# Kernel tuning notes

Hardware: AMD Instinct MI355X
Metric: run time of the kernel (lower is better)

The kernel has to match this reference:

```python
import jax, jax.numpy as jnp
import numpy as np

D = 512
K = 32
B = 2
L = 2048


def setup_inputs() -> dict:
    key = jax.random.key(0)
    ks = jax.random.split(key, 12)
    s = 1.0 / np.sqrt(D)
    return {
        "x": jax.random.normal(ks[0], (B, L, D), dtype=jnp.float32),
        "W1": jax.random.normal(ks[1], (D, D), dtype=jnp.float32) * s,
        "b1": jnp.zeros((D,), jnp.float32),
        "W2": jax.random.normal(ks[2], (D, K), dtype=jnp.float32) * s,
        "b2": jnp.zeros((K,), jnp.float32),
        "pos_scale": jnp.array([0.5], jnp.float32),
        "content_scale": jnp.array([0.5], jnp.float32),
        "Wv": jax.random.normal(ks[3], (D, D), dtype=jnp.float32) * s,
        "bv": jnp.zeros((D,), jnp.float32),
        "ln_g": jnp.ones((D,), jnp.float32),
        "ln_b": jnp.zeros((D,), jnp.float32),
        "Wo": jax.random.normal(ks[4], (D, D), dtype=jnp.float32) * s,
        "bo": jnp.zeros((D,), jnp.float32),
    }


def reference(x, W1, b1, W2, b2, pos_scale, content_scale, Wv, bv, ln_g, ln_b, Wo, bo):
    Bb, Ll, Dd = x.shape
    Kk = W2.shape[1]
    # fixed positional phases: outer(positions, 1/10000^(k/K))
    freqs = 1.0 / (10000.0 ** (jnp.arange(Kk, dtype=jnp.float32) / Kk))
    pos_phase = jnp.arange(Ll, dtype=jnp.float32)[:, None] * freqs[None, :]  # [L,K]
    # content phase: Linear -> Tanh -> Linear, then tanh * pi
    h = jnp.tanh(x @ W1 + b1)
    content_phase = jnp.tanh(h @ W2 + b2) * jnp.pi  # [B,L,K]
    total_phase = pos_scale * pos_phase[None] + content_scale * content_phase  # [B,L,K]
    value = x @ Wv + bv  # [B,L,D]
    c = jnp.cos(total_phase)
    s = jnp.sin(total_phase)
    # phasor outer-product bind: [B,L,K,D]
    bound_real = c[..., None] * value[:, :, None, :]
    bound_imag = s[..., None] * value[:, :, None, :]
    mem_real = jnp.cumsum(bound_real, axis=1)
    mem_imag = jnp.cumsum(bound_imag, axis=1)
    retrieved = (mem_real * c[..., None] + mem_imag * s[..., None]).sum(axis=2)  # [B,L,D]
    norm = jnp.sqrt(jnp.arange(1, Ll + 1, dtype=jnp.float32) * Kk)[None, :, None]
    retrieved = retrieved / norm
    # to_out: LayerNorm then Linear
    mu = retrieved.mean(axis=-1, keepdims=True)
    var = retrieved.var(axis=-1, keepdims=True)
    ln = (retrieved - mu) / jnp.sqrt(var + 1e-5) * ln_g + ln_b
    return x + ln @ Wo + bo
```

## Files before the change

### kernel.cpp

```cpp
#include <hip/hip_runtime.h>
#include <hip/hip_bf16.h>
#include <math.h>

#define BB   2
#define LL   2048
#define DD   512
#define KK   32
#define BL   (BB*LL)
#define NCH  64

typedef unsigned short ushort_t;
typedef __bf16 bf16x8 __attribute__((ext_vector_type(8)));
typedef float  f32x4  __attribute__((ext_vector_type(4)));
typedef unsigned short ushort8 __attribute__((ext_vector_type(8)));

__device__ __forceinline__ void gl_lds16(const void* g, void* l) {
    __builtin_amdgcn_global_load_lds(
        (const __attribute__((address_space(1))) void*)g,
        (__attribute__((address_space(3))) void*)l, 16, 0, 0);
}
__device__ __forceinline__ ushort_t f2b(float f) {
    __bf16 b = (__bf16)f; return *(ushort_t*)&b;
}
__device__ __forceinline__ float b2f(ushort_t u) {
    unsigned int x = ((unsigned int)u) << 16; return *(float*)&x;
}

__global__ __launch_bounds__(256) void prep(const float* __restrict__ W1,
                                            const float* __restrict__ Wv,
                                            const float* __restrict__ Wo,
                                            const float* __restrict__ W2,
                                            const float* __restrict__ x,
                                            const float* __restrict__ lng,
                                            const float* __restrict__ lnb,
                                            const float* __restrict__ bo,
                                            __hip_bfloat16* __restrict__ Wct,
                                            __hip_bfloat16* __restrict__ Wot,
                                            __hip_bfloat16* __restrict__ W2T,
                                            __hip_bfloat16* __restrict__ xb,
                                            float* __restrict__ U,
                                            float* __restrict__ VBc)
{
    __shared__ float tile[32][33];
    const int bz = blockIdx.z;
    const int tx = threadIdx.x, ty = threadIdx.y;
    const int t = ty * 32 + tx;

    if (bz == 3) {
        const int bid = blockIdx.y * 16 + blockIdx.x;
        const float4* src = (const float4*)x + (size_t)bid * 2048 + t;
        ushort4* dst = (ushort4*)xb + (size_t)bid * 2048 + t;
        #pragma unroll
        for (int i = 0; i < 8; ++i) {
            float4 v = src[i * 256];
            ushort4 o = {f2b(v.x), f2b(v.y), f2b(v.z), f2b(v.w)};
            dst[i * 256] = o;
        }
        return;
    }
    if (bz == 4) {
        if (blockIdx.x != 0) return;
        const int kg = blockIdx.y;
        const int k0 = kg * 32;
        float u0 = 0.f, u1 = 0.f, v0 = 0.f, v1 = 0.f;
        #pragma unroll 4
        for (int k = 0; k < 32; ++k) {
            const float g1 = lng[k0 + k], b1v = lnb[k0 + k];
            const float w0 = Wo[(size_t)(k0 + k) * 512 + t];
            const float w1 = Wo[(size_t)(k0 + k) * 512 + t + 256];
            u0 = fmaf(g1, w0, u0);  u1 = fmaf(g1, w1, u1);
            v0 = fmaf(b1v, w0, v0); v1 = fmaf(b1v, w1, v1);
        }
        if (kg == 0) { v0 += bo[t]; v1 += bo[t + 256]; }
        atomicAdd(&U[t], u0);         atomicAdd(&U[t + 256], u1);
        atomicAdd(&VBc[t], v0);       atomicAdd(&VBc[t + 256], v1);
        return;
    }
    if (bz == 5) {
        if (blockIdx.x != 0) return;
        const int r0 = blockIdx.y * 32;
        #pragma unroll
        for (int i = 0; i < 4; ++i)
            tile[ty + 8 * i][tx] = W2[(size_t)(r0 + ty + 8 * i) * 32 + tx];
        __syncthreads();
        #pragma unroll
        for (int i = 0; i < 4; ++i)
            W2T[(size_t)(ty + 8 * i) * 512 + r0 + tx] =
                __float2bfloat16(tile[tx][ty + 8 * i]);
        return;
    }
    const float* src = bz == 0 ? W1 : (bz == 1 ? Wv : Wo);
    __hip_bfloat16* dst = bz == 0 ? Wct
                        : (bz == 1 ? Wct + 512 * 512 : Wot);
    const int r0 = blockIdx.y * 32, c0 = blockIdx.x * 32;
    #pragma unroll
    for (int i = 0; i < 4; ++i)
        tile[ty + 8 * i][tx] = src[(size_t)(r0 + ty + 8 * i) * 512 + c0 + tx];
    __syncthreads();
    const float sc = (bz == 2) ? lng[r0 + tx] : 1.f;
    #pragma unroll
    for (int i = 0; i < 4; ++i)
        dst[(size_t)(c0 + ty + 8 * i) * 512 + r0 + tx] =
            __float2bfloat16(tile[tx][ty + 8 * i] * sc);
}

template<int BM, int MODE>
__global__ __launch_bounds__(256) void gemm_mfma(
    const ushort_t* __restrict__ A, const ushort_t* __restrict__ Bt,
    const float* __restrict__ bias0, const float* __restrict__ bias1,
    const float* __restrict__ resid,
    __hip_bfloat16* __restrict__ outH, __hip_bfloat16* __restrict__ outV,
    float* __restrict__ outF, const float* __restrict__ stats)
{
    constexpr int WROWS = BM / 2;
    constexpr int MF    = WROWS / 16;
    constexpr int ACH   = BM / 32;
    __shared__ __align__(16) ushort_t As[BM * 64];
    __shared__ __align__(16) ushort_t Bs[128 * 64];
    __shared__ float muL[BM], rsL[BM];

    const int t  = threadIdx.x;
    const int m0 = blockIdx.y * BM, n0 = blockIdx.x * 128;
    const int l  = t & 63, w = t >> 6;
    const int wr = w >> 1, wc = w & 1;
    const int l15 = l & 15, hi = l >> 4;

    if (MODE == 1 && t < BM) {
        float4 st = *(const float4*)(stats + (size_t)(m0 + t) * 4);
        float s = st.x + st.z, s2 = st.y + st.w;
        float mu = s * (1.f / 512), var = s2 * (1.f / 512) - mu * mu;
        muL[t] = mu;
        rsL[t] = rsqrtf(var + 1e-5f);
    }

    const ushort_t* agp[ACH];
    const ushort_t* bgp[4];
    #pragma unroll
    for (int i = 0; i < ACH; ++i) {
        int row = (t >> 3) + 32 * i, slot = (t & 7) ^ (row & 7);
        agp[i] = A + (size_t)(m0 + row) * 512 + slot * 8;
    }
    #pragma unroll
    for (int i = 0; i < 4; ++i) {
        int row = (t >> 3) + 32 * i, slot = (t & 7) ^ (row & 7);
        bgp[i] = Bt + (size_t)(n0 + row) * 512 + slot * 8;
    }

    int aoff[MF][2], boff[4][2];
    #pragma unroll
    for (int mi = 0; mi < MF; ++mi)
        #pragma unroll
        for (int kh = 0; kh < 2; ++kh) {
            int row = wr * WROWS + mi * 16 + l15;
            aoff[mi][kh] = row * 128 + (((kh * 4 + hi) ^ (row & 7)) * 16);
        }
    #pragma unroll
    for (int nj = 0; nj < 4; ++nj)
        #pragma unroll
        for (int kh = 0; kh < 2; ++kh) {
            int row = wc * 64 + nj * 16 + l15;
            boff[nj][kh] = row * 128 + (((kh * 4 + hi) ^ (row & 7)) * 16);
        }

    f32x4 acc[MF][4];
    #pragma unroll
    for (int mi = 0; mi < MF; ++mi)
        #pragma unroll
        for (int nj = 0; nj < 4; ++nj)
            acc[mi][nj] = f32x4{0.f, 0.f, 0.f, 0.f};

    for (int k0 = 0; k0 < 512; k0 += 64) {
        __syncthreads();
        #pragma unroll
        for (int i = 0; i < ACH; ++i)
            gl_lds16(agp[i] + k0, (char*)As + (size_t)(i * 256 + t) * 16);
        #pragma unroll
        for (int i = 0; i < 4; ++i)
            gl_lds16(bgp[i] + k0, (char*)Bs + (size_t)(i * 256 + t) * 16);
        __syncthreads();
        #pragma unroll
        for (int kh = 0; kh < 2; ++kh) {
            bf16x8 af[MF], bfr[4];
            #pragma unroll
            for (int mi = 0; mi < MF; ++mi)
                af[mi] = *(const bf16x8*)((const char*)As + aoff[mi][kh]);
            #pragma unroll
            for (int nj = 0; nj < 4; ++nj)
                bfr[nj] = *(const bf16x8*)((const char*)Bs + boff[nj][kh]);
            #pragma unroll
            for (int mi = 0; mi < MF; ++mi)
                #pragma unroll
                for (int nj = 0; nj < 4; ++nj)
                    acc[mi][nj] = __builtin_amdgcn_mfma_f32_16x16x32_bf16(
                        af[mi], bfr[nj], acc[mi][nj], 0, 0, 0);
        }
    }

    #pragma unroll
    for (int nj = 0; nj < 4; ++nj) {
        const int gcol = n0 + wc * 64 + nj * 16 + l15;
        if (MODE == 0) {
            const float bsv = (gcol < 512) ? bias0[gcol] : bias1[gcol - 512];
            #pragma unroll
            for (int mi = 0; mi < MF; ++mi)
                #pragma unroll
                for (int r = 0; r < 4; ++r) {
                    const int grow = m0 + wr * WROWS + mi * 16 + hi * 4 + r;
                    float v = acc[mi][nj][r] + bsv;
                    if (gcol < 512)
                        outH[(size_t)grow * 512 + gcol] = __float2bfloat16(tanhf(v));
                    else
                        outV[(size_t)grow * 512 + (gcol - 512)] = __float2bfloat16(v);
                }
        } else {
            const float uN = bias0[gcol], vbN = bias1[gcol];
            #pragma unroll
            for (int mi = 0; mi < MF; ++mi)
                #pragma unroll
                for (int r = 0; r < 4; ++r) {
                    const int rl = wr * WROWS + mi * 16 + hi * 4 + r;
                    const int grow = m0 + rl;
                    const float rs = rsL[rl], mu = muL[rl];
                    outF[(size_t)grow * 512 + gcol] =
                        resid[(size_t)grow * 512 + gcol]
                        + rs * acc[mi][nj][r] - rs * mu * uN + vbN;
                }
        }
    }
}

__global__ __launch_bounds__(256) void scanA(const __hip_bfloat16* __restrict__ Vb,
                                             const __hip_bfloat16* __restrict__ Hb,
                                             const __hip_bfloat16* __restrict__ W2T,
                                             const float* __restrict__ b2,
                                             const float* __restrict__ ps_p,
                                             const float* __restrict__ cs_p,
                                             float* __restrict__ Ca,
                                             float* __restrict__ Sa,
                                             ushort_t* __restrict__ PPg)
{
    __shared__ __align__(16) ushort_t regA[32 * 520];
    __shared__ __align__(16) ushort_t regB[32 * 520];
    ushort_t* Hs  = regA;
    ushort_t* VT  = regA;
    ushort_t* CT  = regA + 256 * 40;
    ushort_t* ST  = regA + 256 * 40 + 32 * 40;
    ushort_t* W2L = regB;
    ushort_t* PPs = regB;

    const int t = threadIdx.x;
    const int bch = blockIdx.x, dh = blockIdx.y;
    const int b = bch >> 6, ch = bch & 63;
    const size_t vbase = ((size_t)b * LL + ch * 32) * DD + dh * 256;
    const int w = t >> 6, l = t & 63, l15 = l & 15, hi = l >> 4;

    {
        const ushort8* hsrc = (const ushort8*)((const ushort_t*)Hb
                               + ((size_t)b * LL + ch * 32) * DD);
        const ushort8* wsrc = (const ushort8*)((const ushort_t*)W2T);
        #pragma unroll
        for (int i = 0; i < 8; ++i) {
            const int id = i * 256 + t;
            const int row = id >> 6, c8 = id & 63;
            ushort8 hv = hsrc[id];
            ushort8 wv = wsrc[id];
            *(ushort8*)&Hs[row * 520 + c8 * 8] = hv;
            *(ushort8*)&W2L[row * 520 + c8 * 8] = wv;
        }
    }
    __syncthreads();

    f32x4 pacc[2][2];
    #pragma unroll
    for (int mt = 0; mt < 2; ++mt)
        #pragma unroll
        for (int nt = 0; nt < 2; ++nt)
            pacc[mt][nt] = f32x4{0.f,0.f,0.f,0.f};
    for (int ks = 0; ks < 16; ++ks) {
        bf16x8 af[2], bfr[2];
        #pragma unroll
        for (int mt = 0; mt < 2; ++mt)
            af[mt] = *(const bf16x8*)&Hs[(16 * mt + l15) * 520 + ks * 32 + hi * 8];
        #pragma unroll
        for (int nt = 0; nt < 2; ++nt)
            bfr[nt] = *(const bf16x8*)&W2L[(16 * nt + l15) * 520 + ks * 32 + hi * 8];
        #pragma unroll
        for (int mt = 0; mt < 2; ++mt)
            #pragma unroll
            for (int nt = 0; nt < 2; ++nt)
                pacc[mt][nt] = __builtin_amdgcn_mfma_f32_16x16x32_bf16(
                    af[mt], bfr[nt], pacc[mt][nt], 0, 0, 0);
    }
    __syncthreads();

    {
        const float psv = ps_p[0], csv = cs_p[0];
        #pragma unroll
        for (int nt = 0; nt < 2; ++nt) {
            const int kk = l15 + 16 * nt;
            const float freq = exp2f(-(float)kk * (13.287712379549449f / (float)KK));
            const float b2k = b2[kk];
            #pragma unroll
            for (int mt = 0; mt < 2; ++mt) {
                ushort_t cw[4], sw[4];
                #pragma unroll
                for (int r = 0; r < 4; ++r) {
                    const int lloc = 16 * mt + hi * 4 + r;
                    const int lpos = ch * 32 + lloc;
                    const float content = tanhf(pacc[mt][nt][r] + b2k)
                                          * 3.14159265358979323846f * csv;
                    const float total = psv * ((float)lpos * freq) + content;
                    float sv, cv;
                    sincosf(total, &sv, &cv);
                    cw[r] = f2b(cv); sw[r] = f2b(sv);
                    if (dh == 0) {
                        const size_t gi = ((size_t)b * LL + lpos) * KK + kk;
                        Ca[gi] = cv; Sa[gi] = sv;
                    }
                }
                *(ushort4*)&CT[kk * 40 + 16 * mt + hi * 4] = *(ushort4*)cw;
                *(ushort4*)&ST[kk * 40 + 16 * mt + hi * 4] = *(ushort4*)sw;
            }
        }
    }
    {
        const int lg = t >> 5, dg = t & 31;
        ushort8 r[4];
        #pragma unroll
        for (int i = 0; i < 4; ++i)
            r[i] = *(const ushort8*)((const ushort_t*)Vb + vbase
                                     + (size_t)(lg * 4 + i) * DD + dg * 8);
        #pragma unroll
        for (int jd = 0; jd < 8; ++jd) {
            ushort4 w4 = {r[0][jd], r[1][jd], r[2][jd], r[3][jd]};
            *(ushort4*)&VT[(dg * 8 + jd) * 40 + lg * 4] = w4;
        }
    }
    __syncthreads();

    bf16x8 afc[2], afs[2];
    #pragma unroll
    for (int mt = 0; mt < 2; ++mt) {
        afc[mt] = *(const bf16x8*)&CT[(l15 + 16 * mt) * 40 + hi * 8];
        afs[mt] = *(const bf16x8*)&ST[(l15 + 16 * mt) * 40 + hi * 8];
    }
    f32x4 aPR[2][4], aPI[2][4];
    #pragma unroll
    for (int mt = 0; mt < 2; ++mt)
        #pragma unroll
        for (int nt = 0; nt < 4; ++nt) {
            aPR[mt][nt] = f32x4{0.f,0.f,0.f,0.f};
            aPI[mt][nt] = f32x4{0.f,0.f,0.f,0.f};
        }
    #pragma unroll
    for (int nt = 0; nt < 4; ++nt) {
        bf16x8 bv = *(const bf16x8*)&VT[(w * 64 + nt * 16 + l15) * 40 + hi * 8];
        #pragma unroll
        for (int mt = 0; mt < 2; ++mt) {
            aPR[mt][nt] = __builtin_amdgcn_mfma_f32_16x16x32_bf16(afc[mt], bv, aPR[mt][nt], 0,0,0);
            aPI[mt][nt] = __builtin_amdgcn_mfma_f32_16x16x32_bf16(afs[mt], bv, aPI[mt][nt], 0,0,0);
        }
    }
    #pragma unroll
    for (int mt = 0; mt < 2; ++mt)
        #pragma unroll
        for (int nt = 0; nt < 4; ++nt) {
            const int dloc = w * 64 + nt * 16 + l15;
            const int kq = 16 * mt + hi * 4;
            const int oR = kq >> 3, oI = 4 + (kq >> 3);
            const int sub = (hi & 1) * 4;
            ushort4 pr4 = {f2b(aPR[mt][nt][0]), f2b(aPR[mt][nt][1]),
                           f2b(aPR[mt][nt][2]), f2b(aPR[mt][nt][3])};
            ushort4 pi4 = {f2b(aPI[mt][nt][0]), f2b(aPI[mt][nt][1]),
                           f2b(aPI[mt][nt][2]), f2b(aPI[mt][nt][3])};
            *(ushort4*)&PPs[dloc * 64 + ((oR ^ (dloc & 7)) * 8) + sub] = pr4;
            *(ushort4*)&PPs[dloc * 64 + ((oI ^ (dloc & 7)) * 8) + sub] = pi4;
        }
    __syncthreads();
    ushort_t* gout = PPg + ((size_t)bch * 512 + dh * 256) * 64;
    #pragma unroll
    for (int i = 0; i < 8; ++i)
        *(ushort8*)(gout + (size_t)(i * 256 + t) * 8) =
            *(const ushort8*)&PPs[(i * 256 + t) * 8];
}

__global__ __launch_bounds__(256) void scan_prefix(ushort_t* __restrict__ PPg)
{
    const int g = blockIdx.x * 256 + threadIdx.x;
    const int b = g >> 15, p = g & 32767;
    float run = 0.f;
    for (int gg = 0; gg < 4; ++gg) {
        ushort_t v[16];
        #pragma unroll
        for (int i = 0; i < 16; ++i)
            v[i] = PPg[(size_t)(b * 64 + gg * 16 + i) * 32768 + p];
        #pragma unroll
        for (int i = 0; i < 16; ++i) {
            ushort_t o = f2b(run);
            run += b2f(v[i]);
            PPg[(size_t)(b * 64 + gg * 16 + i) * 32768 + p] = o;
        }
    }
}

__global__ __launch_bounds__(256) void scanC(__hip_bfloat16* Vb,
                                             const float* __restrict__ Ca,
                                             const float* __restrict__ Sa,
                                             const ushort_t* __restrict__ PPg,
                                             float* __restrict__ StatsG)
{
    __shared__ __align__(16) ushort_t VT[256 * 40];
    __shared__ __align__(16) ushort_t PPT[256 * 64];
    __shared__ __align__(16) ushort_t CS[32 * 80];
    __shared__ __align__(16) ushort_t G[32 * 40];
    __shared__ __align__(16) ushort_t RT[4][32 * 64];
    __shared__ float2 statsL[4][32];

    const int t = threadIdx.x;
    const int bch = blockIdx.x, dh = blockIdx.y;
    const int b = bch >> 6, ch = bch & 63;
    const size_t vbase = ((size_t)b * LL + ch * 32) * DD + dh * 256;

    {
        const ushort_t* ppg = PPg + ((size_t)bch * 512 + dh * 256) * 64;
        #pragma unroll
        for (int i = 0; i < 8; ++i)
            gl_lds16(ppg + (size_t)(i * 256 + t) * 8,
                     (char*)PPT + (size_t)(i * 256 + t) * 16);
    }
    {
        const int lg = t >> 5, dg = t & 31;
        ushort8 r[4];
        #pragma unroll
        for (int i = 0; i < 4; ++i)
            r[i] = *(const ushort8*)((const ushort_t*)Vb + vbase
                                     + (size_t)(lg * 4 + i) * DD + dg * 8);
        #pragma unroll
        for (int jd = 0; jd < 8; ++jd) {
            ushort4 w4 = {r[0][jd], r[1][jd], r[2][jd], r[3][jd]};
            *(ushort4*)&VT[(dg * 8 + jd) * 40 + lg * 4] = w4;
        }
    }
    {
        const int half = t >> 7;
        const int tt = t & 127;
        const int lrow = tt >> 2, kq = tt & 3;
        const float* srcp = half ? Sa : Ca;
        float4 v0 = *(const float4*)(srcp + ((size_t)b * LL + ch * 32 + lrow) * KK + kq * 8);
        float4 v1 = *(const float4*)(srcp + ((size_t)b * LL + ch * 32 + lrow) * KK + kq * 8 + 4);
        ushort8 w8 = {f2b(v0.x), f2b(v0.y), f2b(v0.z), f2b(v0.w),
                      f2b(v1.x), f2b(v1.y), f2b(v1.z), f2b(v1.w)};
        *(ushort8*)&CS[lrow * 80 + half * 32 + kq * 8] = w8;
    }
    __syncthreads();

    const int w = t >> 6, l = t & 63, l15 = l & 15, hi = l >> 4;

    {
        bf16x8 fc[2], fs[2];
        #pragma unroll
        for (int mt = 0; mt < 2; ++mt) {
            fc[mt] = *(const bf16x8*)&CS[(l15 + 16 * mt) * 80 + hi * 8];
            fs[mt] = *(const bf16x8*)&CS[(l15 + 16 * mt) * 80 + 32 + hi * 8];
        }
        f32x4 gacc[2][2];
        #pragma unroll
        for (int mt = 0; mt < 2; ++mt)
            #pragma unroll
            for (int nt = 0; nt < 2; ++nt) {
                gacc[mt][nt] = f32x4{0.f,0.f,0.f,0.f};
                gacc[mt][nt] = __builtin_amdgcn_mfma_f32_16x16x32_bf16(fc[mt], fc[nt], gacc[mt][nt], 0,0,0);
                gacc[mt][nt] = __builtin_amdgcn_mfma_f32_16x16x32_bf16(fs[mt], fs[nt], gacc[mt][nt], 0,0,0);
            }
        #pragma unroll
        for (int mt = 0; mt < 2; ++mt)
            #pragma unroll
            for (int nt = 0; nt < 2; ++nt)
                #pragma unroll
                for (int r = 0; r < 4; ++r) {
                    const int row = 16 * mt + hi * 4 + r;
                    const int col = 16 * nt + l15;
                    float gv = (col <= row) ? gacc[mt][nt][r] : 0.f;
                    G[row * 40 + col] = f2b(gv);
                }
    }

    bf16x8 a1[2][2], ag[2];
    #pragma unroll
    for (int mt = 0; mt < 2; ++mt) {
        a1[mt][0] = *(const bf16x8*)&CS[(l15 + 16 * mt) * 80 + hi * 8];
        a1[mt][1] = *(const bf16x8*)&CS[(l15 + 16 * mt) * 80 + 32 + hi * 8];
        ag[mt]    = *(const bf16x8*)&G[(l15 + 16 * mt) * 40 + hi * 8];
    }
    f32x4 acc[2][4];
    #pragma unroll
    for (int mt = 0; mt < 2; ++mt)
        #pragma unroll
        for (int nt = 0; nt < 4; ++nt)
            acc[mt][nt] = f32x4{0.f,0.f,0.f,0.f};
    #pragma unroll
    for (int nt = 0; nt < 4; ++nt) {
        const int drow = w * 64 + nt * 16 + l15;
        bf16x8 bp0 = *(const bf16x8*)((const char*)PPT + drow * 128 + ((hi ^ (drow & 7)) << 4));
        bf16x8 bp1 = *(const bf16x8*)((const char*)PPT + drow * 128 + (((4 + hi) ^ (drow & 7)) << 4));
        bf16x8 bv  = *(const bf16x8*)&VT[drow * 40 + hi * 8];
        #pragma unroll
        for (int mt = 0; mt < 2; ++mt) {
            acc[mt][nt] = __builtin_amdgcn_mfma_f32_16x16x32_bf16(a1[mt][0], bp0, acc[mt][nt], 0,0,0);
            acc[mt][nt] = __builtin_amdgcn_mfma_f32_16x16x32_bf16(a1[mt][1], bp1, acc[mt][nt], 0,0,0);
            acc[mt][nt] = __builtin_amdgcn_mfma_f32_16x16x32_bf16(ag[mt],    bv,  acc[mt][nt], 0,0,0);
        }
    }

    float sP[2][4] = {}, qP[2][4] = {};
    #pragma unroll
    for (int mt = 0; mt < 2; ++mt)
        #pragma unroll
        for (int nt = 0; nt < 4; ++nt)
            #pragma unroll
            for (int r = 0; r < 4; ++r) {
                const int lrow = 16 * mt + hi * 4 + r;
                const float scale = rsqrtf((float)((ch * 32 + lrow + 1) * KK));
                const float val = acc[mt][nt][r] * scale;
                sP[mt][r] += val;
                qP[mt][r] = fmaf(val, val, qP[mt][r]);
                RT[w][lrow * 64 + nt * 16 + l15] = f2b(val);
            }
    #pragma unroll
    for (int c = 0; c < 4; ++c) {
        const int cid = c * 64 + l;
        const int row = cid >> 3, c8 = cid & 7;
        ushort8 v = *(const ushort8*)&RT[w][row * 64 + c8 * 8];
        *(ushort8*)((ushort_t*)Vb + ((size_t)b * LL + ch * 32 + row) * DD
                    + dh * 256 + w * 64 + c8 * 8) = v;
    }
    #pragma unroll
    for (int mt = 0; mt < 2; ++mt)
        #pragma unroll
        for (int r = 0; r < 4; ++r) {
            float sv = sP[mt][r], qv = qP[mt][r];
            #pragma unroll
            for (int off = 1; off < 16; off <<= 1) {
                sv += __shfl_xor(sv, off);
                qv += __shfl_xor(qv, off);
            }
            if (l15 == 0)
                statsL[w][16 * mt + hi * 4 + r] = float2{sv, qv};
        }
    __syncthreads();
    if (t < 32) {
        float s = 0.f, q = 0.f;
        #pragma unroll
        for (int w4 = 0; w4 < 4; ++w4) {
            float2 p = statsL[w4][t];
            s += p.x; q += p.y;
        }
        const size_t rowg = (size_t)b * LL + ch * 32 + t;
        *(float2*)&StatsG[(rowg * 2 + dh) * 2] = float2{s, q};
    }
}

extern "C" void kernel_launch(void* const* d_in, const int* in_sizes, int n_in,
                              void* d_out, int out_size, void* d_ws, size_t ws_size,
                              hipStream_t stream)
{
    const float* x   = (const float*)d_in[0];
    const float* W1  = (const float*)d_in[1];
    const float* b1  = (const float*)d_in[2];
    const float* W2  = (const float*)d_in[3];
    const float* b2  = (const float*)d_in[4];
    const float* ps  = (const float*)d_in[5];
    const float* cs  = (const float*)d_in[6];
    const float* Wv  = (const float*)d_in[7];
    const float* bv  = (const float*)d_in[8];
    const float* lng = (const float*)d_in[9];
    const float* lnb = (const float*)d_in[10];
    const float* Wo  = (const float*)d_in[11];
    const float* bo  = (const float*)d_in[12];
    float* out = (float*)d_out;

    char* wsb = (char*)d_ws;
    __hip_bfloat16* Vb  = (__hip_bfloat16*)(wsb);
    ushort_t* PPg = (ushort_t*)(wsb + (4u << 20));
    float* Ca  = (float*)(wsb + (12u << 20));
    float* Sa  = (float*)(wsb + (12u << 20) + (512u << 10));
    __hip_bfloat16* xb  = (__hip_bfloat16*)(wsb + (13u << 20));
    __hip_bfloat16* Hb  = (__hip_bfloat16*)(wsb + (17u << 20));
    __hip_bfloat16* Wct = (__hip_bfloat16*)(wsb + (21u << 20));
    __hip_bfloat16* Wot = (__hip_bfloat16*)(wsb + (22u << 20));
    float* StatsG = (float*)(wsb + (23u << 20));
    float* U      = (float*)(wsb + (23u << 20) + (64u << 10));
    float* VBc    = (float*)(wsb + (23u << 20) + (66u << 10));
    __hip_bfloat16* W2T = (__hip_bfloat16*)(wsb + (23u << 20) + (68u << 10));

    hipMemsetAsync(U, 0, 4096, stream);
    prep<<<dim3(16, 16, 6), dim3(32, 8), 0, stream>>>(
        W1, Wv, Wo, W2, x, lng, lnb, bo, Wct, Wot, W2T, xb, U, VBc);
    gemm_mfma<64, 0><<<dim3(8, 64), dim3(256), 0, stream>>>(
        (const ushort_t*)xb, (const ushort_t*)Wct, b1, bv, nullptr, Hb, Vb, nullptr, nullptr);
    scanA<<<dim3(BB * NCH, 2), dim3(256), 0, stream>>>(
        Vb, Hb, W2T, b2, ps, cs, Ca, Sa, PPg);
    scan_prefix<<<dim3(256), dim3(256), 0, stream>>>(PPg);
    scanC<<<dim3(BB * NCH, 2), dim3(256), 0, stream>>>(Vb, Ca, Sa, PPg, StatsG);
    gemm_mfma<64, 1><<<dim3(4, 64), dim3(256), 0, stream>>>(
        (const ushort_t*)Vb, (const ushort_t*)Wot, U, VBc, x, nullptr, nullptr, out, StatsG);
}
```

Before: 63.67 us.

## Drop memset and atomics, store cos/sin as swizzled bf16, shrink output GEMM tile

The LayerNorm-folded bias vectors are now written as per-group partials and summed inside the output GEMM, which removes the hipMemsetAsync launch and the atomic adds. The cos/sin phases go from scanA to scanC as a pre-swizzled bf16 block that is copied straight into LDS with global_load_lds, instead of two fp32 arrays that needed reloading and converting. The final GEMM switches from 64-row to 32-row tiles, doubling the block count. In exchange, every output GEMM block re-reads 16 partial vectors, and the smaller tiles reuse each loaded Wo tile less.

Result: faster. 59.91 us (-5.9%).

```diff
diff --git a/kernel.cpp b/kernel.cpp
--- a/kernel.cpp
+++ b/kernel.cpp
@@ -38,8 +38,8 @@
                                             __hip_bfloat16* __restrict__ Wot,
                                             __hip_bfloat16* __restrict__ W2T,
                                             __hip_bfloat16* __restrict__ xb,
-                                            float* __restrict__ U,
-                                            float* __restrict__ VBc)
+                                            float* __restrict__ Upart,
+                                            float* __restrict__ Vpart)
 {
     __shared__ float tile[32][33];
     const int bz = blockIdx.z;
@@ -72,8 +72,8 @@
             v0 = fmaf(b1v, w0, v0); v1 = fmaf(b1v, w1, v1);
         }
         if (kg == 0) { v0 += bo[t]; v1 += bo[t + 256]; }
-        atomicAdd(&U[t], u0);         atomicAdd(&U[t + 256], u1);
-        atomicAdd(&VBc[t], v0);       atomicAdd(&VBc[t + 256], v1);
+        Upart[kg * 512 + t] = u0;       Upart[kg * 512 + t + 256] = u1;
+        Vpart[kg * 512 + t] = v0;       Vpart[kg * 512 + t + 256] = v1;
         return;
     }
     if (bz == 5) {
@@ -117,7 +117,7 @@
     constexpr int ACH   = BM / 32;
     __shared__ __align__(16) ushort_t As[BM * 64];
     __shared__ __align__(16) ushort_t Bs[128 * 64];
-    __shared__ float muL[BM], rsL[BM];
+    __shared__ float muL[BM], rsL[BM], uL[128], vbL[128];
 
     const int t  = threadIdx.x;
     const int m0 = blockIdx.y * BM, n0 = blockIdx.x * 128;
@@ -125,12 +125,23 @@
     const int wr = w >> 1, wc = w & 1;
     const int l15 = l & 15, hi = l >> 4;
 
-    if (MODE == 1 && t < BM) {
-        float4 st = *(const float4*)(stats + (size_t)(m0 + t) * 4);
-        float s = st.x + st.z, s2 = st.y + st.w;
-        float mu = s * (1.f / 512), var = s2 * (1.f / 512) - mu * mu;
-        muL[t] = mu;
-        rsL[t] = rsqrtf(var + 1e-5f);
+    if (MODE == 1) {
+        if (t < BM) {
+            float4 st = *(const float4*)(stats + (size_t)(m0 + t) * 4);
+            float s = st.x + st.z, s2 = st.y + st.w;
+            float mu = s * (1.f / 512), var = s2 * (1.f / 512) - mu * mu;
+            muL[t] = mu;
+            rsL[t] = rsqrtf(var + 1e-5f);
+        }
+        if (t < 128) {
+            float u = 0.f, v = 0.f;
+            #pragma unroll
+            for (int kg = 0; kg < 16; ++kg) {
+                u += bias0[kg * 512 + n0 + t];
+                v += bias1[kg * 512 + n0 + t];
+            }
+            uL[t] = u; vbL[t] = v;
+        }
     }
 
     const ushort_t* agp[ACH];
@@ -213,7 +224,8 @@
                         outV[(size_t)grow * 512 + (gcol - 512)] = __float2bfloat16(v);
                 }
         } else {
-            const float uN = bias0[gcol], vbN = bias1[gcol];
+            const int lc = wc * 64 + nj * 16 + l15;
+            const float uN = uL[lc], vbN = vbL[lc];
             #pragma unroll
             for (int mi = 0; mi < MF; ++mi)
                 #pragma unroll
@@ -235,8 +247,7 @@
                                              const float* __restrict__ b2,
                                              const float* __restrict__ ps_p,
                                              const float* __restrict__ cs_p,
-                                             float* __restrict__ Ca,
-                                             float* __restrict__ Sa,
+                                             ushort_t* __restrict__ CSg,
                                              ushort_t* __restrict__ PPg)
 {
     __shared__ __align__(16) ushort_t regA[32 * 520];
@@ -245,6 +256,7 @@
     ushort_t* VT  = regA;
     ushort_t* CT  = regA + 256 * 40;
     ushort_t* ST  = regA + 256 * 40 + 32 * 40;
+    ushort_t* CSs = regA + 256 * 40 + 2 * 32 * 40;
     ushort_t* W2L = regB;
     ushort_t* PPs = regB;
 
@@ -314,8 +326,8 @@
                     sincosf(total, &sv, &cv);
                     cw[r] = f2b(cv); sw[r] = f2b(sv);
                     if (dh == 0) {
-                        const size_t gi = ((size_t)b * LL + lpos) * KK + kk;
-                        Ca[gi] = cv; Sa[gi] = sv;
+                        CSs[lloc * 64 + (((kk >> 3) ^ (lloc & 7)) << 3) + (kk & 7)] = cw[r];
+                        CSs[lloc * 64 + ((((kk >> 3) + 4) ^ (lloc & 7)) << 3) + (kk & 7)] = sw[r];
                     }
                 }
                 *(ushort4*)&CT[kk * 40 + 16 * mt + hi * 4] = *(ushort4*)cw;
@@ -337,6 +349,11 @@
         }
     }
     __syncthreads();
+
+    if (dh == 0) {
+        ushort_t* cso = CSg + ((size_t)b * NCH + ch) * 2048;
+        *(ushort8*)(cso + t * 8) = *(const ushort8*)&CSs[t * 8];
+    }
 
     bf16x8 afc[2], afs[2];
     #pragma unroll
@@ -404,14 +421,13 @@
 }
 
 __global__ __launch_bounds__(256) void scanC(__hip_bfloat16* Vb,
-                                             const float* __restrict__ Ca,
-                                             const float* __restrict__ Sa,
+                                             const ushort_t* __restrict__ CSg,
                                              const ushort_t* __restrict__ PPg,
                                              float* __restrict__ StatsG)
 {
     __shared__ __align__(16) ushort_t VT[256 * 40];
     __shared__ __align__(16) ushort_t PPT[256 * 64];
-    __shared__ __align__(16) ushort_t CS[32 * 80];
+    __shared__ __align__(16) ushort_t CS[32 * 64];
     __shared__ __align__(16) ushort_t G[32 * 40];
     __shared__ __align__(16) ushort_t RT[4][32 * 64];
     __shared__ float2 statsL[4][32];
@@ -427,6 +443,8 @@
         for (int i = 0; i < 8; ++i)
             gl_lds16(ppg + (size_t)(i * 256 + t) * 8,
                      (char*)PPT + (size_t)(i * 256 + t) * 16);
+        const ushort_t* csg = CSg + ((size_t)b * NCH + ch) * 2048;
+        gl_lds16(csg + (size_t)t * 8, (char*)CS + (size_t)t * 16);
     }
     {
         const int lg = t >> 5, dg = t & 31;
@@ -441,28 +459,19 @@
             *(ushort4*)&VT[(dg * 8 + jd) * 40 + lg * 4] = w4;
         }
     }
+    __syncthreads();
+
+    const int w = t >> 6, l = t & 63, l15 = l & 15, hi = l >> 4;
+
+    bf16x8 fc[2], fs[2];
+    #pragma unroll
+    for (int mt = 0; mt < 2; ++mt) {
+        const int row = l15 + 16 * mt;
+        fc[mt] = *(const bf16x8*)&CS[row * 64 + ((hi ^ (row & 7)) << 3)];
+        fs[mt] = *(const bf16x8*)&CS[row * 64 + (((4 + hi) ^ (row & 7)) << 3)];
+    }
+
     {
-        const int half = t >> 7;
-        const int tt = t & 127;
-        const int lrow = tt >> 2, kq = tt & 3;
-        const float* srcp = half ? Sa : Ca;
-        float4 v0 = *(const float4*)(srcp + ((size_t)b * LL + ch * 32 + lrow) * KK + kq * 8);
-        float4 v1 = *(const float4*)(srcp + ((size_t)b * LL + ch * 32 + lrow) * KK + kq * 8 + 4);
-        ushort8 w8 = {f2b(v0.x), f2b(v0.y), f2b(v0.z), f2b(v0.w),
-                      f2b(v1.x), f2b(v1.y), f2b(v1.z), f2b(v1.w)};
-        *(ushort8*)&CS[lrow * 80 + half * 32 + kq * 8] = w8;
-    }
-    __syncthreads();
-
-    const int w = t >> 6, l = t & 63, l15 = l & 15, hi = l >> 4;
-
-    {
-        bf16x8 fc[2], fs[2];
-        #pragma unroll
-        for (int mt = 0; mt < 2; ++mt) {
-            fc[mt] = *(const bf16x8*)&CS[(l15 + 16 * mt) * 80 + hi * 8];
-            fs[mt] = *(const bf16x8*)&CS[(l15 + 16 * mt) * 80 + 32 + hi * 8];
-        }
         f32x4 gacc[2][2];
         #pragma unroll
         for (int mt = 0; mt < 2; ++mt)
@@ -485,13 +494,11 @@
                 }
     }
 
-    bf16x8 a1[2][2], ag[2];
-    #pragma unroll
-    for (int mt = 0; mt < 2; ++mt) {
-        a1[mt][0] = *(const bf16x8*)&CS[(l15 + 16 * mt) * 80 + hi * 8];
-        a1[mt][1] = *(const bf16x8*)&CS[(l15 + 16 * mt) * 80 + 32 + hi * 8];
-        ag[mt]    = *(const bf16x8*)&G[(l15 + 16 * mt) * 40 + hi * 8];
-    }
+    bf16x8 ag[2];
+    #pragma unroll
+    for (int mt = 0; mt < 2; ++mt)
+        ag[mt] = *(const bf16x8*)&G[(l15 + 16 * mt) * 40 + hi * 8];
+
     f32x4 acc[2][4];
     #pragma unroll
     for (int mt = 0; mt < 2; ++mt)
@@ -506,9 +513,9 @@
         bf16x8 bv  = *(const bf16x8*)&VT[drow * 40 + hi * 8];
         #pragma unroll
         for (int mt = 0; mt < 2; ++mt) {
-            acc[mt][nt] = __builtin_amdgcn_mfma_f32_16x16x32_bf16(a1[mt][0], bp0, acc[mt][nt], 0,0,0);
-            acc[mt][nt] = __builtin_amdgcn_mfma_f32_16x16x32_bf16(a1[mt][1], bp1, acc[mt][nt], 0,0,0);
-            acc[mt][nt] = __builtin_amdgcn_mfma_f32_16x16x32_bf16(ag[mt],    bv,  acc[mt][nt], 0,0,0);
+            acc[mt][nt] = __builtin_amdgcn_mfma_f32_16x16x32_bf16(fc[mt], bp0, acc[mt][nt], 0,0,0);
+            acc[mt][nt] = __builtin_amdgcn_mfma_f32_16x16x32_bf16(fs[mt], bp1, acc[mt][nt], 0,0,0);
+            acc[mt][nt] = __builtin_amdgcn_mfma_f32_16x16x32_bf16(ag[mt], bv,  acc[mt][nt], 0,0,0);
         }
     }
 
@@ -582,26 +589,24 @@
     char* wsb = (char*)d_ws;
     __hip_bfloat16* Vb  = (__hip_bfloat16*)(wsb);
     ushort_t* PPg = (ushort_t*)(wsb + (4u << 20));
-    float* Ca  = (float*)(wsb + (12u << 20));
-    float* Sa  = (float*)(wsb + (12u << 20) + (512u << 10));
+    ushort_t* CSg = (ushort_t*)(wsb + (12u << 20));
     __hip_bfloat16* xb  = (__hip_bfloat16*)(wsb + (13u << 20));
     __hip_bfloat16* Hb  = (__hip_bfloat16*)(wsb + (17u << 20));
     __hip_bfloat16* Wct = (__hip_bfloat16*)(wsb + (21u << 20));
     __hip_bfloat16* Wot = (__hip_bfloat16*)(wsb + (22u << 20));
     float* StatsG = (float*)(wsb + (23u << 20));
-    float* U      = (float*)(wsb + (23u << 20) + (64u << 10));
-    float* VBc    = (float*)(wsb + (23u << 20) + (66u << 10));
-    __hip_bfloat16* W2T = (__hip_bfloat16*)(wsb + (23u << 20) + (68u << 10));
-
-    hipMemsetAsync(U, 0, 4096, stream);
+    float* Upart  = (float*)(wsb + (23u << 20) + (64u << 10));
+    float* Vpart  = (float*)(wsb + (23u << 20) + (96u << 10));
+    __hip_bfloat16* W2T = (__hip_bfloat16*)(wsb + (23u << 20) + (128u << 10));
+
     prep<<<dim3(16, 16, 6), dim3(32, 8), 0, stream>>>(
-        W1, Wv, Wo, W2, x, lng, lnb, bo, Wct, Wot, W2T, xb, U, VBc);
+        W1, Wv, Wo, W2, x, lng, lnb, bo, Wct, Wot, W2T, xb, Upart, Vpart);
     gemm_mfma<64, 0><<<dim3(8, 64), dim3(256), 0, stream>>>(
         (const ushort_t*)xb, (const ushort_t*)Wct, b1, bv, nullptr, Hb, Vb, nullptr, nullptr);
     scanA<<<dim3(BB * NCH, 2), dim3(256), 0, stream>>>(
-        Vb, Hb, W2T, b2, ps, cs, Ca, Sa, PPg);
+        Vb, Hb, W2T, b2, ps, cs, CSg, PPg);
     scan_prefix<<<dim3(256), dim3(256), 0, stream>>>(PPg);
-    scanC<<<dim3(BB * NCH, 2), dim3(256), 0, stream>>>(Vb, Ca, Sa, PPg, StatsG);
-    gemm_mfma<64, 1><<<dim3(4, 64), dim3(256), 0, stream>>>(
-        (const ushort_t*)Vb, (const ushort_t*)Wot, U, VBc, x, nullptr, nullptr, out, StatsG);
-}
+    scanC<<<dim3(BB * NCH, 2), dim3(256), 0, stream>>>(Vb, CSg, PPg, StatsG);
+    gemm_mfma<32, 1><<<dim3(4, 128), dim3(256), 0, stream>>>(
+        (const ushort_t*)Vb, (const ushort_t*)Wot, Upart, Vpart, x, nullptr, nullptr, out, StatsG);
+}
```
